# Kernel optimization log

Measured on AMD Instinct MI355X. Metric: run time of the kernel, lower is better.

The kernel has to match this reference:

```python
import jax, jax.numpy as jnp
import numpy as np

B, K, C = 1024, 8, 10   # predicted points, concepts, classes per concept
N = 8192                # background (training) set size
EPS = 1e-13


def setup_inputs() -> dict:
    key = jax.random.key(0)
    k1, k2, k3 = jax.random.split(key, 3)
    c_p = jax.random.normal(k1, (B, K, C), dtype=jnp.float32)
    bandwidth = jnp.ones((K * C,), dtype=jnp.float32)  # learned param, init 1.0
    c_in = jax.random.randint(k2, (N, K), 0, C, dtype=jnp.int64)
    delta_in = jax.random.randint(k3, (N,), 0, 2, dtype=jnp.int32)
    return {"c_p": c_p, "bandwidth": bandwidth, "c_in": c_in, "delta_in": delta_in}


def _beran(c_p, bandwidth, c_in, delta_in):
    # ---- GaussKernel l2 metric ----
    proba = jax.nn.softmax(c_p, axis=-1)                      # [B,K,C]
    bw = jnp.clip(bandwidth, 0.001, 10.0).reshape(K, C)       # [K,C]
    onehot = jax.nn.one_hot(c_in, C, dtype=proba.dtype)       # [N,K,C]
    # sum((p - l)^2 / bw) = sum(p^2/bw) - 2 sum(p*l/bw) + sum(l^2/bw)
    A = jnp.sum(proba * proba / bw, axis=(1, 2))              # [B]
    D = jnp.einsum('nkc,kc->n', onehot, 1.0 / bw)             # [N]
    cross = jnp.einsum('bkc,nkc->bn', proba / bw, onehot)     # [B,N]
    metric = A[:, None] - 2.0 * cross + D[None, :]            # [B,N]
    weights = jnp.exp(-metric)
    s = jnp.sum(weights, axis=1, keepdims=True)               # normalize over background axis
    bad = s < EPS
    W = jnp.where(bad, 0.0, weights / jnp.where(bad, 1.0, s)) # [B,N]

    # ---- Beran cumulative hazard scan ----
    w_cumsum = jnp.cumsum(W, axis=1)
    shifted = w_cumsum - W
    ones = jnp.ones_like(shifted)
    bad2 = jnp.isclose(shifted, ones) | jnp.isclose(w_cumsum, ones)
    shifted = jnp.where(bad2, 0.0, shifted)
    w_cumsum = jnp.where(bad2, 0.0, w_cumsum)
    xi = jnp.log(1.0 - shifted) - jnp.log(1.0 - w_cumsum)
    filtered_xi = delta_in.astype(xi.dtype)[None, :] * xi
    hazards = jnp.cumsum(filtered_xi, axis=1)
    surv_func = jnp.exp(-hazards)                             # [B,N]
    first_step = 1.0 - surv_func[:, :1]
    surv_steps = jnp.concatenate([first_step, surv_func[:, :-1] - surv_func[:, 1:]], axis=1)
    ss = jnp.sum(surv_steps, axis=1, keepdims=True)
    bad3 = ss < EPS
    surv_steps = jnp.where(bad3, 0.0, surv_steps / jnp.where(bad3, 1.0, ss))
    return surv_func, surv_steps


def reference(c_p, bandwidth, c_in, delta_in):
    return _beran(c_p, bandwidth, c_in, delta_in)
```

## Files before the change

### kernel.cpp

```cpp
#include <hip/hip_runtime.h>

#define NN 8192
#define BB 1024
#define KK 8
#define CC 10
#define NT 512
#define CHUNK (NN/NT)
#define NW (NT/64)
#define T3SZ 2100
#define HALF 4096

__device__ __forceinline__ int swz(int n) {
    return (n & ~31) | ((n + (n >> 5)) & 31);
}

__global__ void pack_kernel(const int* __restrict__ c_in, const int* __restrict__ delta_in,
                            unsigned* __restrict__ pairs, unsigned* __restrict__ dmask_g) {
    int n = blockIdx.x * blockDim.x + threadIdx.x;
    if (n >= NN) return;
    const int4* p = reinterpret_cast<const int4*>(c_in + (size_t)n * KK);
    int4 lo = p[0], hi = p[1];
    unsigned g0 = (unsigned)((lo.x * 10 + lo.y) * 10 + lo.z);
    unsigned g1 = (unsigned)((lo.w * 10 + hi.x) * 10 + hi.y);
    unsigned g2 = (unsigned)(hi.z * 10 + hi.w);
    pairs[n] = g0 | (g1 << 10) | (g2 << 20);
    unsigned long long bal = __ballot(delta_in[n] & 1);
    if ((threadIdx.x & 63) == 0) {
        dmask_g[n >> 5]       = (unsigned)(bal & 0xffffffffull);
        dmask_g[(n >> 5) + 1] = (unsigned)(bal >> 32);
    }
}

__global__ __launch_bounds__(NT, 8) void beran_kernel(
    const float* __restrict__ c_p, const float* __restrict__ bandwidth,
    const int* __restrict__ c_in, const int* __restrict__ delta_in,
    const unsigned* __restrict__ pairs, const unsigned* __restrict__ dmask_g,
    float* __restrict__ out)
{
    __shared__ float a2[HALF];
    __shared__ float tb[KK * CC];
    __shared__ float Apart[KK];
    __shared__ float t3[T3SZ];
    __shared__ float wsA[NW];
    __shared__ float wsM[NW];
    __shared__ float s4095;

    const int b    = blockIdx.x;
    const int t    = threadIdx.x;
    const int lane = t & 63;
    const int wv   = t >> 6;
    const int base = t * CHUNK;

    if (t < KK) {
        const int k = t;
        float v[CC];
        float mx = -1e30f;
        #pragma unroll
        for (int c = 0; c < CC; c++) { v[c] = c_p[((size_t)b*KK + k)*CC + c]; mx = fmaxf(mx, v[c]); }
        float se = 0.0f;
        #pragma unroll
        for (int c = 0; c < CC; c++) { v[c] = __expf(v[c] - mx); se += v[c]; }
        float inv = 1.0f / se;
        float Ak = 0.0f;
        #pragma unroll
        for (int c = 0; c < CC; c++) {
            float p  = v[c] * inv;
            float bw = bandwidth[k*CC + c];
            bw = fminf(fmaxf(bw, 0.001f), 10.0f);
            float ib = 1.0f / bw;
            tb[k*CC + c] = ib - 2.0f * p * ib;
            Ak += p * p * ib;
        }
        Apart[k] = Ak;
    }
    __syncthreads();

    for (int i = t; i < T3SZ; i += NT) {
        float v;
        if (i < 1000) {
            v = tb[0*CC + i/100] + tb[1*CC + (i/10)%10] + tb[2*CC + i%10];
        } else if (i < 2000) {
            int j = i - 1000;
            v = tb[3*CC + j/100] + tb[4*CC + (j/10)%10] + tb[5*CC + j%10];
        } else {
            int q = i - 2000;
            float Ar = 0.0f;
            #pragma unroll
            for (int k = 0; k < KK; k++) Ar += Apart[k];
            v = tb[6*CC + q/10] + tb[7*CC + q%10] + Ar;
        }
        t3[i] = -v;
    }
    __syncthreads();

    float creg[CHUNK];
    unsigned dm = 0;
    float run = 0.0f;
    if (pairs) {
        dm = (dmask_g[t >> 1] >> ((t & 1) * 16)) & 0xffffu;
        #pragma unroll
        for (int g = 0; g < CHUNK / 4; g++) {
            uint4 v = *reinterpret_cast<const uint4*>(pairs + base + g * 4);
#define DO3(w0, idx) { \
            float m = t3[(w0) & 1023] + t3[1000 + (((w0) >> 10) & 1023)] \
                    + t3[2000 + ((w0) >> 20)]; \
            run += __expf(m); creg[idx] = run; }
            DO3(v.x, g*4 + 0)
            DO3(v.y, g*4 + 1)
            DO3(v.z, g*4 + 2)
            DO3(v.w, g*4 + 3)
#undef DO3
        }
    } else {
        float A = 0.0f;
        #pragma unroll
        for (int k = 0; k < KK; k++) A += Apart[k];
        #pragma unroll
        for (int i = 0; i < CHUNK; i++) {
            const int4* p4 = reinterpret_cast<const int4*>(c_in + (size_t)(base + i) * KK);
            int4 lo = p4[0], hi = p4[1];
            float m = A;
            m += tb[0*CC + lo.x] + tb[1*CC + lo.y] + tb[2*CC + lo.z] + tb[3*CC + lo.w];
            m += tb[4*CC + hi.x] + tb[5*CC + hi.y] + tb[6*CC + hi.z] + tb[7*CC + hi.w];
            run += __expf(-m);
            creg[i] = run;
            dm |= (unsigned)(delta_in[base + i] & 1) << i;
        }
    }

    float x = run;
    #pragma unroll
    for (int d = 1; d < 64; d <<= 1) {
        float y = __shfl_up(x, d);
        if (lane >= d) x += y;
    }
    if (lane == 63) wsA[wv] = x;
    __syncthreads();
    float s = 0.0f, woff = 0.0f;
    #pragma unroll
    for (int w = 0; w < NW; w++) {
        float y = wsA[w];
        s += y;
        if (w < wv) woff += y;
    }
    const float off_raw = woff + (x - run);
    const float invs = (s < 1e-13f) ? 0.0f : 1.0f / s;

    const float ISO = 1.00001e-5f;
    float uprev = 1.0f - off_raw * invs;
    float P = 1.0f;
    #pragma unroll
    for (int i = 0; i < CHUNK; i++) {
        float cs = (creg[i] + off_raw) * invs;
        float u  = 1.0f - cs;
        bool bad  = (fabsf(uprev) <= ISO) || (fabsf(u) <= ISO);
        bool flag = (dm >> i) & 1u;
        float f = (flag && !bad) ? u * __builtin_amdgcn_rcpf(uprev) : 1.0f;
        P *= f;
        creg[i] = P;
        uprev = u;
    }

    float xm = P;
    #pragma unroll
    for (int d = 1; d < 64; d <<= 1) {
        float y = __shfl_up(xm, d);
        if (lane >= d) xm *= y;
    }
    if (lane == 63) wsM[wv] = xm;
    __syncthreads();
    float tot = 1.0f, moff = 1.0f;
    #pragma unroll
    for (int w = 0; w < NW; w++) {
        float y = wsM[w];
        tot *= y;
        if (w < wv) moff *= y;
    }
    float exclm = __shfl_up(xm, 1);
    if (lane == 0) exclm = 1.0f;
    const float S_base = moff * exclm;

    #pragma unroll
    for (int i = 0; i < CHUNK; i++) creg[i] = S_base * creg[i];
    if (t == NT/2) s4095 = S_base;

    const float ss = 1.0f - tot;
    const float invss = (ss < 1e-13f) ? 0.0f : 1.0f / ss;
    float* outS = out + (size_t)b * NN;
    float* outT = out + (size_t)BB * NN + (size_t)b * NN;

    #pragma unroll
    for (int sidx = 0; sidx < 2; sidx++) {
        __syncthreads();
        if ((t >> 8) == sidx) {
            const int lb = base - sidx * HALF;
            #pragma unroll
            for (int i = 0; i < CHUNK; i++) a2[swz(lb + i)] = creg[i];
        }
        __syncthreads();
        #pragma unroll
        for (int j = 0; j < 2; j++) {
            const int nl = j * 2048 + t * 4;
            const int n0 = sidx * HALF + nl;
            float s0 = a2[swz(nl)];
            float s1 = a2[swz(nl + 1)];
            float s2 = a2[swz(nl + 2)];
            float s3 = a2[swz(nl + 3)];
            float sp = (nl == 0) ? ((sidx == 0) ? 1.0f : s4095) : a2[swz(nl - 1)];
            *reinterpret_cast<float4*>(outS + n0) = make_float4(s0, s1, s2, s3);
            *reinterpret_cast<float4*>(outT + n0) =
                make_float4((sp - s0) * invss, (s0 - s1) * invss,
                            (s1 - s2) * invss, (s2 - s3) * invss);
        }
    }
}

extern "C" void kernel_launch(void* const* d_in, const int* in_sizes, int n_in,
                              void* d_out, int out_size, void* d_ws, size_t ws_size,
                              hipStream_t stream) {
    const float* c_p       = (const float*)d_in[0];
    const float* bandwidth = (const float*)d_in[1];
    const int*   c_in      = (const int*)d_in[2];
    const int*   delta_in  = (const int*)d_in[3];
    float* out = (float*)d_out;

    unsigned* pairs   = nullptr;
    unsigned* dmask_g = nullptr;
    const size_t need = (size_t)NN * sizeof(unsigned) + (size_t)(NN / 32) * sizeof(unsigned);
    if (ws_size >= need) {
        pairs   = (unsigned*)d_ws;
        dmask_g = (unsigned*)((char*)d_ws + (size_t)NN * sizeof(unsigned));
        pack_kernel<<<NN / 256, 256, 0, stream>>>(c_in, delta_in, pairs, dmask_g);
    }
    beran_kernel<<<BB, NT, 0, stream>>>(c_p, bandwidth, c_in, delta_in, pairs, dmask_g, out);
}
```

Before: 28.05 us.

## Prefetch packed codes early, parallelize softmax prep, use nontemporal stores, drop a barrier

The packed code words and the delta mask are now loaded at kernel entry, before the softmax setup, so global load latency overlaps the prologue. The softmax/bandwidth preparation is spread over 80 threads (one per concept-class) instead of 8, each recomputing its row max and sum. Output stores become nontemporal, and the barrier ordering the two half-buffer passes is restructured so one fewer barrier runs. The cost is redundant per-thread exp work in the prologue, early-live registers, and reliance on a correct barrier placement for shared buffer reuse.

```diff
diff --git a/kernel.cpp b/kernel.cpp
--- a/kernel.cpp
+++ b/kernel.cpp
@@ -9,6 +9,8 @@
 #define NW (NT/64)
 #define T3SZ 2100
 #define HALF 4096
+
+typedef float f32x4 __attribute__((ext_vector_type(4)));
 
 __device__ __forceinline__ int swz(int n) {
     return (n & ~31) | ((n + (n >> 5)) & 31);
@@ -39,7 +41,7 @@
 {
     __shared__ float a2[HALF];
     __shared__ float tb[KK * CC];
-    __shared__ float Apart[KK];
+    __shared__ float psc[KK * CC];
     __shared__ float t3[T3SZ];
     __shared__ float wsA[NW];
     __shared__ float wsM[NW];
@@ -51,27 +53,32 @@
     const int wv   = t >> 6;
     const int base = t * CHUNK;
 
-    if (t < KK) {
-        const int k = t;
-        float v[CC];
-        float mx = -1e30f;
-        #pragma unroll
-        for (int c = 0; c < CC; c++) { v[c] = c_p[((size_t)b*KK + k)*CC + c]; mx = fmaxf(mx, v[c]); }
-        float se = 0.0f;
-        #pragma unroll
-        for (int c = 0; c < CC; c++) { v[c] = __expf(v[c] - mx); se += v[c]; }
-        float inv = 1.0f / se;
-        float Ak = 0.0f;
-        #pragma unroll
-        for (int c = 0; c < CC; c++) {
-            float p  = v[c] * inv;
-            float bw = bandwidth[k*CC + c];
-            bw = fminf(fmaxf(bw, 0.001f), 10.0f);
-            float ib = 1.0f / bw;
-            tb[k*CC + c] = ib - 2.0f * p * ib;
-            Ak += p * p * ib;
-        }
-        Apart[k] = Ak;
+    uint4 u0, u1, u2, u3;
+    unsigned dm32 = 0;
+    if (pairs) {
+        const uint4* pp = reinterpret_cast<const uint4*>(pairs + base);
+        u0 = pp[0]; u1 = pp[1]; u2 = pp[2]; u3 = pp[3];
+        dm32 = dmask_g[t >> 1];
+    }
+
+    if (t < KK * CC) {
+        const int k = t / CC, c = t - (t / CC) * CC;
+        const float* row = c_p + ((size_t)b * KK + k) * CC;
+        float mx = row[0];
+        #pragma unroll
+        for (int j = 1; j < CC; j++) mx = fmaxf(mx, row[j]);
+        float se = 0.0f, ec = 0.0f;
+        #pragma unroll
+        for (int j = 0; j < CC; j++) {
+            float e = __expf(row[j] - mx);
+            se += e;
+            if (j == c) ec = e;
+        }
+        float p  = ec * (1.0f / se);
+        float bw = fminf(fmaxf(bandwidth[k * CC + c], 0.001f), 10.0f);
+        float ib = 1.0f / bw;
+        tb[t]  = ib - 2.0f * p * ib;
+        psc[t] = p * p * ib;
     }
     __syncthreads();
 
@@ -86,7 +93,7 @@
             int q = i - 2000;
             float Ar = 0.0f;
             #pragma unroll
-            for (int k = 0; k < KK; k++) Ar += Apart[k];
+            for (int e = 0; e < KK * CC; e++) Ar += psc[e];
             v = tb[6*CC + q/10] + tb[7*CC + q%10] + Ar;
         }
         t3[i] = -v;
@@ -97,24 +104,20 @@
     unsigned dm = 0;
     float run = 0.0f;
     if (pairs) {
-        dm = (dmask_g[t >> 1] >> ((t & 1) * 16)) & 0xffffu;
-        #pragma unroll
-        for (int g = 0; g < CHUNK / 4; g++) {
-            uint4 v = *reinterpret_cast<const uint4*>(pairs + base + g * 4);
+        dm = (dm32 >> ((t & 1) * 16)) & 0xffffu;
 #define DO3(w0, idx) { \
-            float m = t3[(w0) & 1023] + t3[1000 + (((w0) >> 10) & 1023)] \
-                    + t3[2000 + ((w0) >> 20)]; \
-            run += __expf(m); creg[idx] = run; }
-            DO3(v.x, g*4 + 0)
-            DO3(v.y, g*4 + 1)
-            DO3(v.z, g*4 + 2)
-            DO3(v.w, g*4 + 3)
+        float m = t3[(w0) & 1023] + t3[1000 + (((w0) >> 10) & 1023)] \
+                + t3[2000 + ((w0) >> 20)]; \
+        run += __expf(m); creg[idx] = run; }
+        DO3(u0.x,  0) DO3(u0.y,  1) DO3(u0.z,  2) DO3(u0.w,  3)
+        DO3(u1.x,  4) DO3(u1.y,  5) DO3(u1.z,  6) DO3(u1.w,  7)
+        DO3(u2.x,  8) DO3(u2.y,  9) DO3(u2.z, 10) DO3(u2.w, 11)
+        DO3(u3.x, 12) DO3(u3.y, 13) DO3(u3.z, 14) DO3(u3.w, 15)
 #undef DO3
-        }
     } else {
         float A = 0.0f;
         #pragma unroll
-        for (int k = 0; k < KK; k++) A += Apart[k];
+        for (int e = 0; e < KK * CC; e++) A += psc[e];
         #pragma unroll
         for (int i = 0; i < CHUNK; i++) {
             const int4* p4 = reinterpret_cast<const int4*>(c_in + (size_t)(base + i) * KK);
@@ -191,7 +194,6 @@
 
     #pragma unroll
     for (int sidx = 0; sidx < 2; sidx++) {
-        __syncthreads();
         if ((t >> 8) == sidx) {
             const int lb = base - sidx * HALF;
             #pragma unroll
@@ -207,11 +209,13 @@
             float s2 = a2[swz(nl + 2)];
             float s3 = a2[swz(nl + 3)];
             float sp = (nl == 0) ? ((sidx == 0) ? 1.0f : s4095) : a2[swz(nl - 1)];
-            *reinterpret_cast<float4*>(outS + n0) = make_float4(s0, s1, s2, s3);
-            *reinterpret_cast<float4*>(outT + n0) =
-                make_float4((sp - s0) * invss, (s0 - s1) * invss,
-                            (s1 - s2) * invss, (s2 - s3) * invss);
-        }
+            f32x4 ov = {s0, s1, s2, s3};
+            f32x4 st = {(sp - s0) * invss, (s0 - s1) * invss,
+                        (s1 - s2) * invss, (s2 - s3) * invss};
+            __builtin_nontemporal_store(ov, reinterpret_cast<f32x4*>(outS + n0));
+            __builtin_nontemporal_store(st, reinterpret_cast<f32x4*>(outT + n0));
+        }
+        if (sidx == 0) __syncthreads();
     }
 }
 
```

Result: slower. 28.69 us (+2.3%).
